# Optimization experiments

Hardware: AMD Instinct MI355X
Metric: run time of the kernel (lower is better)

Reference implementation:

```python
import jax, jax.numpy as jnp
import numpy as np

B, E, H, V, D2, T = 128, 512, 512, 32000, 1024, 17

def setup_inputs() -> dict:
    key = jax.random.key(0)
    ks = jax.random.split(key, 13)
    s = 0.02
    return {
        "features": jax.random.normal(ks[0], (B, 512), dtype=jnp.float32),
        "captions": jax.random.randint(ks[1], (B, T), 0, V, dtype=jnp.int32),
        "W_enc": jax.random.normal(ks[2], (512, E), dtype=jnp.float32) * s,
        "b_enc": jnp.zeros((E,), dtype=jnp.float32),
        "emb": jax.random.normal(ks[3], (V, E), dtype=jnp.float32) * s,
        "W_ih": jax.random.normal(ks[4], (4 * H, E), dtype=jnp.float32) * s,
        "b_ih": jnp.zeros((4 * H,), dtype=jnp.float32),
        "W_hh": jax.random.normal(ks[5], (4 * H, H), dtype=jnp.float32) * s,
        "b_hh": jnp.zeros((4 * H,), dtype=jnp.float32),
        "W_d2": jax.random.normal(ks[6], (H, D2), dtype=jnp.float32) * s,
        "b_d2": jnp.zeros((D2,), dtype=jnp.float32),
        "W_last": jax.random.normal(ks[7], (D2, V), dtype=jnp.float32) * s,
        "b_last": jnp.zeros((V,), dtype=jnp.float32),
    }


def reference(features, captions, W_enc, b_enc, emb, W_ih, b_ih, W_hh, b_hh, W_d2, b_d2, W_last, b_last):
    # encoder_last: project frozen-resnet features [B,512] -> [B,E]
    feat = features @ W_enc + b_enc
    # embed captions[:, :-1] -> [B,16,E], prepend image feature -> [B,17,E]
    e = emb[captions[:, :-1]]
    x = jnp.concatenate([feat[:, None, :], e], axis=1)  # [B,T,E]

    def step(carry, xt):
        h, c = carry
        gates = xt @ W_ih.T + b_ih + h @ W_hh.T + b_hh  # [B,4H]
        i, f, g, o = jnp.split(gates, 4, axis=-1)  # PyTorch LSTMCell gate order
        i, f, o = jax.nn.sigmoid(i), jax.nn.sigmoid(f), jax.nn.sigmoid(o)
        g = jnp.tanh(g)
        c = f * c + i * g
        h = o * jnp.tanh(c)
        return (h, c), h

    h0 = jnp.zeros((x.shape[0], H), dtype=x.dtype)
    c0 = jnp.zeros((x.shape[0], H), dtype=x.dtype)
    _, hs = jax.lax.scan(step, (h0, c0), jnp.swapaxes(x, 0, 1))  # [T,B,H]
    hs = jnp.swapaxes(hs, 0, 1)  # [B,T,H]

    out = jax.nn.relu(hs @ W_d2 + b_d2)       # [B,T,D2]
    logits = out @ W_last + b_last            # [B,T,V]
    return jax.nn.softmax(logits, axis=2)
```

## Files before the change

### kernel.cpp

```cpp
#include <hip/hip_runtime.h>
#include <hip/hip_bf16.h>

#define B_   128
#define T_   17
#define E_   512
#define H_   512
#define V_   32000
#define D2_  1024
#define MR_  (B_*T_)

typedef __attribute__((ext_vector_type(8))) short short8;
typedef __attribute__((ext_vector_type(4))) float f32x4;

__device__ __forceinline__ unsigned short f2b(float f) {
  unsigned u = __float_as_uint(f);
  u += 0x7FFFu + ((u >> 16) & 1u);
  return (unsigned short)(u >> 16);
}

__device__ __forceinline__ void async16(const void* g, void* l) {
  __builtin_amdgcn_global_load_lds((const __attribute__((address_space(1))) unsigned int*)g,
                                   (__attribute__((address_space(3))) unsigned int*)l,
                                   16, 0, 0);
}

template<int EPI>
__global__ __launch_bounds__(256, 2)
void gemm_bt(const unsigned short* __restrict__ A,
             const unsigned short* __restrict__ Bt,
             void* __restrict__ C,
             const float* __restrict__ bias0,
             const float* __restrict__ bias1,
             int N, int K)
{
  __shared__ unsigned short sA[128 * 32];
  __shared__ unsigned short sB[128 * 32];

  const int tid  = threadIdx.x;
  const int lane = tid & 63;
  const int wave = tid >> 6;
  const int wm   = wave & 1;
  const int wn   = wave >> 1;
  const size_t bm = (size_t)blockIdx.y * 128;
  const size_t bn = (size_t)blockIdx.x * 128;

  const int sRow   = wave * 32 + (lane >> 2);
  const int cpos   = lane & 3;
  const int gchunk = cpos ^ (sRow & 3);

  const unsigned short* gA  = A  + (bm + sRow)      * (size_t)K + gchunk * 8;
  const unsigned short* gA2 = A  + (bm + sRow + 16) * (size_t)K + gchunk * 8;
  const unsigned short* gB  = Bt + (bn + sRow)      * (size_t)K + gchunk * 8;
  const unsigned short* gB2 = Bt + (bn + sRow + 16) * (size_t)K + gchunk * 8;

  unsigned short* lA  = &sA[wave * 1024];
  unsigned short* lA2 = &sA[wave * 1024 + 512];
  unsigned short* lB  = &sB[wave * 1024];
  unsigned short* lB2 = &sB[wave * 1024 + 512];

  f32x4 acc[4][4] = {};

  const int fm = lane & 15;
  const int q  = lane >> 4;

  for (int kt = 0; kt < K; kt += 32) {
    async16(gA  + kt, lA);
    async16(gA2 + kt, lA2);
    async16(gB  + kt, lB);
    async16(gB2 + kt, lB2);
    __syncthreads();

    short8 af[4], bfv[4];
#pragma unroll
    for (int i = 0; i < 4; i++) {
      int ra = wm * 64 + i * 16 + fm;
      af[i]  = *(const short8*)&sA[ra * 32 + ((q ^ (ra & 3)) * 8)];
      int rb = wn * 64 + i * 16 + fm;
      bfv[i] = *(const short8*)&sB[rb * 32 + ((q ^ (rb & 3)) * 8)];
    }
#pragma unroll
    for (int i = 0; i < 4; i++)
#pragma unroll
      for (int j = 0; j < 4; j++)
        acc[i][j] = __builtin_amdgcn_mfma_f32_16x16x32_bf16(af[i], bfv[j], acc[i][j], 0, 0, 0);
    __syncthreads();
  }

#pragma unroll
  for (int i = 0; i < 4; i++) {
#pragma unroll
    for (int j = 0; j < 4; j++) {
      size_t col = bn + wn * 64 + j * 16 + fm;
      float bv = 0.f;
      if constexpr (EPI == 0) bv = bias0[col] + bias1[col];
      if constexpr (EPI == 2 || EPI == 3) bv = bias0[col];
#pragma unroll
      for (int r = 0; r < 4; r++) {
        size_t row = bm + wm * 64 + i * 16 + q * 4 + r;
        float v = acc[i][j][r] + bv;
        if constexpr (EPI == 2) {
          v = v > 0.f ? v : 0.f;
          ((unsigned short*)C)[row * N + col] = f2b(v);
        } else {
          ((float*)C)[row * N + col] = v;
        }
      }
    }
  }
}

__global__ void cvt_bf16(const float* __restrict__ src, unsigned short* __restrict__ dst, int n4) {
  int i = blockIdx.x * 256 + threadIdx.x;
  if (i >= n4) return;
  float4 v = ((const float4*)src)[i];
  ushort4 o;
  o.x = f2b(v.x); o.y = f2b(v.y); o.z = f2b(v.z); o.w = f2b(v.w);
  ((ushort4*)dst)[i] = o;
}

__global__ void transpose_cvt(const float* __restrict__ src, unsigned short* __restrict__ dst,
                              int K, int N) {
  __shared__ float tile[32][33];
  int n0 = blockIdx.x * 32, k0 = blockIdx.y * 32;
  int tcol = threadIdx.x & 31, trow = threadIdx.x >> 5;
  for (int r = trow; r < 32; r += 8)
    tile[r][tcol] = src[(size_t)(k0 + r) * N + n0 + tcol];
  __syncthreads();
  for (int r = trow; r < 32; r += 8)
    dst[(size_t)(n0 + r) * K + k0 + tcol] = f2b(tile[tcol][r]);
}

__global__ __launch_bounds__(256) void encode(const float* __restrict__ features,
                                              const float* __restrict__ W_enc,
                                              const float* __restrict__ b_enc,
                                              unsigned short* __restrict__ xb) {
  __shared__ float fs[512];
  int b = blockIdx.y, e = blockIdx.x * 256 + threadIdx.x;
  fs[threadIdx.x]       = features[b * 512 + threadIdx.x];
  fs[threadIdx.x + 256] = features[b * 512 + threadIdx.x + 256];
  __syncthreads();
  float acc = 0.f;
#pragma unroll 8
  for (int k = 0; k < 512; k++) acc += fs[k] * W_enc[(size_t)k * 512 + e];
  xb[(size_t)b * 512 + e] = f2b(acc + b_enc[e]);
}

__global__ void embed_k(const int* __restrict__ captions, const float* __restrict__ emb,
                        unsigned short* __restrict__ xb) {
  int t = blockIdx.x + 1, b = blockIdx.y;
  int tok = captions[b * T_ + (t - 1)];
  float4 v = ((const float4*)(emb + (size_t)tok * 512))[threadIdx.x];
  ushort4 o;
  o.x = f2b(v.x); o.y = f2b(v.y); o.z = f2b(v.z); o.w = f2b(v.w);
  ((ushort4*)(xb + (size_t)(t * B_ + b) * 512))[threadIdx.x] = o;
}

__global__ void lstm_point(const float* __restrict__ Gt, const float* __restrict__ lin,
                           float* __restrict__ c, unsigned short* __restrict__ hb,
                           unsigned short* __restrict__ hsb, int t, int has_lin) {
  int idx = blockIdx.x * 256 + threadIdx.x;
  int b = idx >> 9, j = idx & 511;
  const float* g = Gt + (size_t)b * 2048;
  float gi = g[j], gf = g[512 + j], gg = g[1024 + j], go = g[1536 + j];
  if (has_lin) {
    const float* l = lin + (size_t)b * 2048;
    gi += l[j]; gf += l[512 + j]; gg += l[1024 + j]; go += l[1536 + j];
  }
  float ii = 1.f / (1.f + __expf(-gi));
  float ff = 1.f / (1.f + __expf(-gf));
  float oo = 1.f / (1.f + __expf(-go));
  float gt = tanhf(gg);
  float cprev = has_lin ? c[idx] : 0.f;
  float cn = ff * cprev + ii * gt;
  float hn = oo * tanhf(cn);
  c[idx] = cn;
  unsigned short h16 = f2b(hn);
  hb[idx] = h16;
  hsb[((size_t)b * T_ + t) * 512 + j] = h16;
}

__global__ __launch_bounds__(1024) void softmax_k(float* __restrict__ out) {
  __shared__ float ps[1024];
  float* r = out + (size_t)blockIdx.x * V_;
  int tid = threadIdx.x;
  float v[32];
  float s = 0.f;
#pragma unroll
  for (int u = 0; u < 32; u++) {
    int i = u * 1024 + tid;
    if (i < V_) { float e = __expf(r[i]); v[u] = e; s += e; }
  }
  ps[tid] = s;
  __syncthreads();
  for (int o = 512; o > 0; o >>= 1) {
    if (tid < o) ps[tid] += ps[tid + o];
    __syncthreads();
  }
  float inv = 1.f / ps[0];
#pragma unroll
  for (int u = 0; u < 32; u++) {
    int i = u * 1024 + tid;
    if (i < V_) r[i] = v[u] * inv;
  }
}

extern "C" void kernel_launch(void* const* d_in, const int* in_sizes, int n_in,
                              void* d_out, int out_size, void* d_ws, size_t ws_size,
                              hipStream_t stream) {
  const float* features = (const float*)d_in[0];
  const int*   captions = (const int*)d_in[1];
  const float* W_enc  = (const float*)d_in[2];
  const float* b_enc  = (const float*)d_in[3];
  const float* emb    = (const float*)d_in[4];
  const float* W_ih   = (const float*)d_in[5];
  const float* b_ih   = (const float*)d_in[6];
  const float* W_hh   = (const float*)d_in[7];
  const float* b_hh   = (const float*)d_in[8];
  const float* W_d2   = (const float*)d_in[9];
  const float* b_d2   = (const float*)d_in[10];
  const float* W_last = (const float*)d_in[11];
  const float* b_last = (const float*)d_in[12];
  float* out = (float*)d_out;

  char* ws = (char*)d_ws;
  size_t off = 0;
  auto alloc = [&](size_t bytes) -> void* {
    void* p = ws + off;
    off += (bytes + 255) & ~(size_t)255;
    return p;
  };
  unsigned short* xb     = (unsigned short*)alloc((size_t)MR_ * E_ * 2);
  unsigned short* Wb_ih  = (unsigned short*)alloc((size_t)4 * H_ * E_ * 2);
  unsigned short* Wb_hh  = (unsigned short*)alloc((size_t)4 * H_ * H_ * 2);
  unsigned short* Wb_d2t = (unsigned short*)alloc((size_t)D2_ * H_ * 2);
  unsigned short* Wb_lt  = (unsigned short*)alloc((size_t)V_ * D2_ * 2);
  float*          G      = (float*)alloc((size_t)MR_ * 4 * H_ * 4);
  float*          lin    = (float*)alloc((size_t)B_ * 4 * H_ * 4);
  float*          cst    = (float*)alloc((size_t)B_ * H_ * 4);
  unsigned short* hb     = (unsigned short*)alloc((size_t)B_ * H_ * 2);
  unsigned short* hsb    = (unsigned short*)alloc((size_t)MR_ * H_ * 2);
  unsigned short* outb   = (unsigned short*)alloc((size_t)MR_ * D2_ * 2);
  (void)in_sizes; (void)n_in; (void)out_size; (void)ws_size;

  cvt_bf16<<<(4 * H_ * E_ / 4 + 255) / 256, 256, 0, stream>>>(W_ih, Wb_ih, 4 * H_ * E_ / 4);
  cvt_bf16<<<(4 * H_ * H_ / 4 + 255) / 256, 256, 0, stream>>>(W_hh, Wb_hh, 4 * H_ * H_ / 4);
  transpose_cvt<<<dim3(D2_ / 32, H_ / 32), 256, 0, stream>>>(W_d2, Wb_d2t, H_, D2_);
  transpose_cvt<<<dim3(V_ / 32, D2_ / 32), 256, 0, stream>>>(W_last, Wb_lt, D2_, V_);

  encode<<<dim3(2, B_), 256, 0, stream>>>(features, W_enc, b_enc, xb);
  embed_k<<<dim3(T_ - 1, B_), 128, 0, stream>>>(captions, emb, xb);

  gemm_bt<0><<<dim3(4 * H_ / 128, MR_ / 128), 256, 0, stream>>>(xb, Wb_ih, G, b_ih, b_hh, 4 * H_, E_);

  lstm_point<<<B_ * H_ / 256, 256, 0, stream>>>(G, nullptr, cst, hb, hsb, 0, 0);
  for (int t = 1; t < T_; t++) {
    gemm_bt<1><<<dim3(4 * H_ / 128, 1), 256, 0, stream>>>(hb, Wb_hh, lin, nullptr, nullptr, 4 * H_, H_);
    lstm_point<<<B_ * H_ / 256, 256, 0, stream>>>(G + (size_t)t * B_ * 4 * H_, lin, cst, hb, hsb, t, 1);
  }

  gemm_bt<2><<<dim3(D2_ / 128, MR_ / 128), 256, 0, stream>>>(hsb, Wb_d2t, outb, b_d2, nullptr, D2_, H_);

  gemm_bt<3><<<dim3(V_ / 128, MR_ / 128), 256, 0, stream>>>(outb, Wb_lt, out, b_last, nullptr, V_, D2_);

  softmax_k<<<MR_, 1024, 0, stream>>>(out);
}
```

Before: 1.022 ms.

## Fuse LSTM recurrence GEMM with cell update, interleave gates, store bf16 logits

Replaces the per-step recurrent GEMM plus pointwise kernel pair with a single fused lstm_step kernel. It uses gate-interleaved weight rows so each block computes all four gates for its hidden units, and double-buffers h. It also swaps the grid so blocks walk M fastest for weight reuse, changes the LDS swizzle, and uses a faster tanh. Logits are written as bf16 to a workspace buffer when space allows, which halves the write and read traffic of the large vocabulary output before softmax. Rounding the logits to bf16 before exp adds precision error.

```diff
diff --git a/kernel.cpp b/kernel.cpp
--- a/kernel.cpp
+++ b/kernel.cpp
@@ -16,6 +16,12 @@
   unsigned u = __float_as_uint(f);
   u += 0x7FFFu + ((u >> 16) & 1u);
   return (unsigned short)(u >> 16);
+}
+__device__ __forceinline__ float sigf(float x) { return 1.f / (1.f + __expf(-x)); }
+__device__ __forceinline__ float tanhfast(float x) {
+  x = fminf(fmaxf(x, -15.f), 15.f);
+  float e = __expf(2.f * x);
+  return (e - 1.f) / (e + 1.f);
 }
 
 __device__ __forceinline__ void async16(const void* g, void* l) {
@@ -41,12 +47,11 @@
   const int wave = tid >> 6;
   const int wm   = wave & 1;
   const int wn   = wave >> 1;
-  const size_t bm = (size_t)blockIdx.y * 128;
-  const size_t bn = (size_t)blockIdx.x * 128;
+  const size_t bm = (size_t)blockIdx.x * 128;
+  const size_t bn = (size_t)blockIdx.y * 128;
 
   const int sRow   = wave * 32 + (lane >> 2);
-  const int cpos   = lane & 3;
-  const int gchunk = cpos ^ (sRow & 3);
+  const int gchunk = (lane & 3) ^ ((sRow >> 2) & 3);
 
   const unsigned short* gA  = A  + (bm + sRow)      * (size_t)K + gchunk * 8;
   const unsigned short* gA2 = A  + (bm + sRow + 16) * (size_t)K + gchunk * 8;
@@ -59,7 +64,6 @@
   unsigned short* lB2 = &sB[wave * 1024 + 512];
 
   f32x4 acc[4][4] = {};
-
   const int fm = lane & 15;
   const int q  = lane >> 4;
 
@@ -74,9 +78,9 @@
 #pragma unroll
     for (int i = 0; i < 4; i++) {
       int ra = wm * 64 + i * 16 + fm;
-      af[i]  = *(const short8*)&sA[ra * 32 + ((q ^ (ra & 3)) * 8)];
+      af[i]  = *(const short8*)&sA[ra * 32 + ((q ^ ((ra >> 2) & 3)) * 8)];
       int rb = wn * 64 + i * 16 + fm;
-      bfv[i] = *(const short8*)&sB[rb * 32 + ((q ^ (rb & 3)) * 8)];
+      bfv[i] = *(const short8*)&sB[rb * 32 + ((q ^ ((rb >> 2) & 3)) * 8)];
     }
 #pragma unroll
     for (int i = 0; i < 4; i++)
@@ -92,8 +96,11 @@
     for (int j = 0; j < 4; j++) {
       size_t col = bn + wn * 64 + j * 16 + fm;
       float bv = 0.f;
-      if constexpr (EPI == 0) bv = bias0[col] + bias1[col];
-      if constexpr (EPI == 2 || EPI == 3) bv = bias0[col];
+      if constexpr (EPI == 0) {
+        size_t oc = ((col & 3) << 9) + (col >> 2);
+        bv = bias0[oc] + bias1[oc];
+      }
+      if constexpr (EPI == 2 || EPI == 3 || EPI == 4) bv = bias0[col];
 #pragma unroll
       for (int r = 0; r < 4; r++) {
         size_t row = bm + wm * 64 + i * 16 + q * 4 + r;
@@ -101,6 +108,8 @@
         if constexpr (EPI == 2) {
           v = v > 0.f ? v : 0.f;
           ((unsigned short*)C)[row * N + col] = f2b(v);
+        } else if constexpr (EPI == 3) {
+          ((unsigned short*)C)[row * N + col] = f2b(v);
         } else {
           ((float*)C)[row * N + col] = v;
         }
@@ -109,13 +118,113 @@
   }
 }
 
-__global__ void cvt_bf16(const float* __restrict__ src, unsigned short* __restrict__ dst, int n4) {
-  int i = blockIdx.x * 256 + threadIdx.x;
-  if (i >= n4) return;
-  float4 v = ((const float4*)src)[i];
+__global__ __launch_bounds__(256)
+void lstm_step(const unsigned short* __restrict__ hprev,
+               const unsigned short* __restrict__ Whh,
+               const float* __restrict__ Gt,
+               float* __restrict__ c,
+               unsigned short* __restrict__ hout,
+               unsigned short* __restrict__ hsb,
+               int t)
+{
+  __shared__ float gl[128 * 132];
+  unsigned short* sA = (unsigned short*)gl;
+  unsigned short* sB = (unsigned short*)(gl + 4096);
+
+  const int tid  = threadIdx.x;
+  const int lane = tid & 63;
+  const int wave = tid >> 6;
+  const int wm   = wave & 1;
+  const int wn   = wave >> 1;
+  const int n0   = blockIdx.x * 128;
+
+  const int sR  = lane >> 3;
+  const int gch = (lane & 7) ^ sR;
+  const size_t aoff = (size_t)(wave * 32 + sR) * 512 + gch * 8;
+  const size_t boff = (size_t)(n0 + wave * 32 + sR) * 512 + gch * 8;
+
+  f32x4 acc[4][4] = {};
+  const int fm = lane & 15;
+  const int q  = lane >> 4;
+
+  for (int kt = 0; kt < 512; kt += 64) {
+#pragma unroll
+    for (int s = 0; s < 4; s++) {
+      async16(hprev + aoff + s * 4096 + kt, sA + wave * 2048 + s * 512);
+      async16(Whh   + boff + s * 4096 + kt, sB + wave * 2048 + s * 512);
+    }
+    __syncthreads();
+
+    short8 af[2][4], bfv[2][4];
+#pragma unroll
+    for (int kk = 0; kk < 2; kk++) {
+      int cch = kk * 4 + q;
+#pragma unroll
+      for (int i = 0; i < 4; i++) {
+        int ra = wm * 64 + i * 16 + fm;
+        af[kk][i]  = *(const short8*)&sA[ra * 64 + ((cch ^ (ra & 7)) * 8)];
+        int rb = wn * 64 + i * 16 + fm;
+        bfv[kk][i] = *(const short8*)&sB[rb * 64 + ((cch ^ (rb & 7)) * 8)];
+      }
+    }
+#pragma unroll
+    for (int kk = 0; kk < 2; kk++)
+#pragma unroll
+      for (int i = 0; i < 4; i++)
+#pragma unroll
+        for (int j = 0; j < 4; j++)
+          acc[i][j] = __builtin_amdgcn_mfma_f32_16x16x32_bf16(af[kk][i], bfv[kk][j], acc[i][j], 0, 0, 0);
+    __syncthreads();
+  }
+
+#pragma unroll
+  for (int i = 0; i < 4; i++)
+#pragma unroll
+    for (int j = 0; j < 4; j++)
+#pragma unroll
+      for (int r = 0; r < 4; r++)
+        gl[(wm * 64 + i * 16 + q * 4 + r) * 132 + wn * 64 + j * 16 + fm] = acc[i][j][r];
+  __syncthreads();
+
+#pragma unroll
+  for (int it = 0; it < 16; it++) {
+    int p   = it * 256 + tid;
+    int row = p >> 5;
+    int ul  = p & 31;
+    float4 a4 = *(float4*)&gl[row * 132 + ul * 4];
+    float4 G4 = *(const float4*)&Gt[row * 2048 + n0 + ul * 4];
+    float gi = a4.x + G4.x, gf = a4.y + G4.y, gg = a4.z + G4.z, go = a4.w + G4.w;
+    int gu  = (n0 >> 2) + ul;
+    int idx = row * 512 + gu;
+    float cn = sigf(gf) * c[idx] + sigf(gi) * tanhfast(gg);
+    c[idx] = cn;
+    float hn = sigf(go) * tanhfast(cn);
+    unsigned short h16 = f2b(hn);
+    hout[idx] = h16;
+    hsb[((size_t)row * T_ + t) * 512 + gu] = h16;
+  }
+}
+
+__global__ void lstm_point0(const float* __restrict__ G0, float* __restrict__ c,
+                            unsigned short* __restrict__ hb, unsigned short* __restrict__ hsb) {
+  int idx = blockIdx.x * 256 + threadIdx.x;
+  int b = idx >> 9, u = idx & 511;
+  float4 g4 = ((const float4*)(G0 + (size_t)b * 2048))[u];
+  float cn = sigf(g4.x) * tanhfast(g4.z);
+  c[idx] = cn;
+  float hn = sigf(g4.w) * tanhfast(cn);
+  unsigned short h16 = f2b(hn);
+  hb[idx] = h16;
+  hsb[((size_t)b * T_ + 0) * 512 + u] = h16;
+}
+
+__global__ void permute_cvt(const float* __restrict__ src, unsigned short* __restrict__ dst) {
+  int p  = blockIdx.x;
+  int ir = ((p & 3) << 9) + (p >> 2);
+  float4 v = ((const float4*)(src + (size_t)ir * 512))[threadIdx.x];
   ushort4 o;
   o.x = f2b(v.x); o.y = f2b(v.y); o.z = f2b(v.z); o.w = f2b(v.w);
-  ((ushort4*)dst)[i] = o;
+  ((ushort4*)(dst + (size_t)p * 512))[threadIdx.x] = o;
 }
 
 __global__ void transpose_cvt(const float* __restrict__ src, unsigned short* __restrict__ dst,
@@ -155,31 +264,50 @@
   ((ushort4*)(xb + (size_t)(t * B_ + b) * 512))[threadIdx.x] = o;
 }
 
-__global__ void lstm_point(const float* __restrict__ Gt, const float* __restrict__ lin,
-                           float* __restrict__ c, unsigned short* __restrict__ hb,
-                           unsigned short* __restrict__ hsb, int t, int has_lin) {
-  int idx = blockIdx.x * 256 + threadIdx.x;
-  int b = idx >> 9, j = idx & 511;
-  const float* g = Gt + (size_t)b * 2048;
-  float gi = g[j], gf = g[512 + j], gg = g[1024 + j], go = g[1536 + j];
-  if (has_lin) {
-    const float* l = lin + (size_t)b * 2048;
-    gi += l[j]; gf += l[512 + j]; gg += l[1024 + j]; go += l[1536 + j];
-  }
-  float ii = 1.f / (1.f + __expf(-gi));
-  float ff = 1.f / (1.f + __expf(-gf));
-  float oo = 1.f / (1.f + __expf(-go));
-  float gt = tanhf(gg);
-  float cprev = has_lin ? c[idx] : 0.f;
-  float cn = ff * cprev + ii * gt;
-  float hn = oo * tanhf(cn);
-  c[idx] = cn;
-  unsigned short h16 = f2b(hn);
-  hb[idx] = h16;
-  hsb[((size_t)b * T_ + t) * 512 + j] = h16;
-}
-
-__global__ __launch_bounds__(1024) void softmax_k(float* __restrict__ out) {
+__global__ __launch_bounds__(1024) void softmax_b(const unsigned short* __restrict__ lg,
+                                                  float* __restrict__ out) {
+  __shared__ float ps[1024];
+  const uint4* r4 = (const uint4*)(lg + (size_t)blockIdx.x * V_);
+  float* orow = out + (size_t)blockIdx.x * V_;
+  int tid = threadIdx.x;
+  float v[4][8];
+  float s = 0.f;
+#pragma unroll
+  for (int u = 0; u < 4; u++) {
+    int i = u * 1024 + tid;
+    if (i < 4000) {
+      uint4 w = r4[i];
+      unsigned a[4] = {w.x, w.y, w.z, w.w};
+#pragma unroll
+      for (int k = 0; k < 4; k++) {
+        float lo = __uint_as_float(a[k] << 16);
+        float hi = __uint_as_float(a[k] & 0xffff0000u);
+        float e0 = __expf(lo), e1 = __expf(hi);
+        v[u][2 * k] = e0; v[u][2 * k + 1] = e1;
+        s += e0 + e1;
+      }
+    }
+  }
+  ps[tid] = s;
+  __syncthreads();
+  for (int o = 512; o > 0; o >>= 1) {
+    if (tid < o) ps[tid] += ps[tid + o];
+    __syncthreads();
+  }
+  float inv = 1.f / ps[0];
+#pragma unroll
+  for (int u = 0; u < 4; u++) {
+    int i = u * 1024 + tid;
+    if (i < 4000) {
+      float4 o1 = {v[u][0] * inv, v[u][1] * inv, v[u][2] * inv, v[u][3] * inv};
+      float4 o2 = {v[u][4] * inv, v[u][5] * inv, v[u][6] * inv, v[u][7] * inv};
+      ((float4*)(orow + (size_t)i * 8))[0] = o1;
+      ((float4*)(orow + (size_t)i * 8))[1] = o2;
+    }
+  }
+}
+
+__global__ __launch_bounds__(1024) void softmax_f(float* __restrict__ out) {
   __shared__ float ps[1024];
   float* r = out + (size_t)blockIdx.x * V_;
   int tid = threadIdx.x;
@@ -235,32 +363,41 @@
   unsigned short* Wb_d2t = (unsigned short*)alloc((size_t)D2_ * H_ * 2);
   unsigned short* Wb_lt  = (unsigned short*)alloc((size_t)V_ * D2_ * 2);
   float*          G      = (float*)alloc((size_t)MR_ * 4 * H_ * 4);
-  float*          lin    = (float*)alloc((size_t)B_ * 4 * H_ * 4);
   float*          cst    = (float*)alloc((size_t)B_ * H_ * 4);
-  unsigned short* hb     = (unsigned short*)alloc((size_t)B_ * H_ * 2);
+  unsigned short* hb0    = (unsigned short*)alloc((size_t)B_ * H_ * 2);
+  unsigned short* hb1    = (unsigned short*)alloc((size_t)B_ * H_ * 2);
   unsigned short* hsb    = (unsigned short*)alloc((size_t)MR_ * H_ * 2);
   unsigned short* outb   = (unsigned short*)alloc((size_t)MR_ * D2_ * 2);
-  (void)in_sizes; (void)n_in; (void)out_size; (void)ws_size;
-
-  cvt_bf16<<<(4 * H_ * E_ / 4 + 255) / 256, 256, 0, stream>>>(W_ih, Wb_ih, 4 * H_ * E_ / 4);
-  cvt_bf16<<<(4 * H_ * H_ / 4 + 255) / 256, 256, 0, stream>>>(W_hh, Wb_hh, 4 * H_ * H_ / 4);
+  size_t off_base = off;
+  unsigned short* lgb    = (unsigned short*)alloc((size_t)MR_ * V_ * 2);
+  const bool bf16_logits = (off <= ws_size);
+  (void)in_sizes; (void)n_in; (void)out_size; (void)off_base;
+
+  permute_cvt<<<2048, 128, 0, stream>>>(W_ih, Wb_ih);
+  permute_cvt<<<2048, 128, 0, stream>>>(W_hh, Wb_hh);
   transpose_cvt<<<dim3(D2_ / 32, H_ / 32), 256, 0, stream>>>(W_d2, Wb_d2t, H_, D2_);
-  transpose_cvt<<<dim3(V_ / 32, D2_ / 32), 256, 0, stream>>>(W_last, Wb_lt, D2_, V_);
 
   encode<<<dim3(2, B_), 256, 0, stream>>>(features, W_enc, b_enc, xb);
   embed_k<<<dim3(T_ - 1, B_), 128, 0, stream>>>(captions, emb, xb);
 
-  gemm_bt<0><<<dim3(4 * H_ / 128, MR_ / 128), 256, 0, stream>>>(xb, Wb_ih, G, b_ih, b_hh, 4 * H_, E_);
-
-  lstm_point<<<B_ * H_ / 256, 256, 0, stream>>>(G, nullptr, cst, hb, hsb, 0, 0);
+  gemm_bt<0><<<dim3(MR_ / 128, 4 * H_ / 128), 256, 0, stream>>>(xb, Wb_ih, G, b_ih, b_hh, 4 * H_, E_);
+
+  lstm_point0<<<B_ * H_ / 256, 256, 0, stream>>>(G, cst, hb0, hsb);
   for (int t = 1; t < T_; t++) {
-    gemm_bt<1><<<dim3(4 * H_ / 128, 1), 256, 0, stream>>>(hb, Wb_hh, lin, nullptr, nullptr, 4 * H_, H_);
-    lstm_point<<<B_ * H_ / 256, 256, 0, stream>>>(G + (size_t)t * B_ * 4 * H_, lin, cst, hb, hsb, t, 1);
-  }
-
-  gemm_bt<2><<<dim3(D2_ / 128, MR_ / 128), 256, 0, stream>>>(hsb, Wb_d2t, outb, b_d2, nullptr, D2_, H_);
-
-  gemm_bt<3><<<dim3(V_ / 128, MR_ / 128), 256, 0, stream>>>(outb, Wb_lt, out, b_last, nullptr, V_, D2_);
-
-  softmax_k<<<MR_, 1024, 0, stream>>>(out);
-}
+    unsigned short* hp = (t & 1) ? hb0 : hb1;
+    unsigned short* hc = (t & 1) ? hb1 : hb0;
+    lstm_step<<<16, 256, 0, stream>>>(hp, Wb_hh, G + (size_t)t * B_ * 4 * H_, cst, hc, hsb, t);
+  }
+
+  transpose_cvt<<<dim3(V_ / 32, D2_ / 32), 256, 0, stream>>>(W_last, Wb_lt, D2_, V_);
+
+  gemm_bt<2><<<dim3(MR_ / 128, D2_ / 128), 256, 0, stream>>>(hsb, Wb_d2t, outb, b_d2, nullptr, D2_, H_);
+
+  if (bf16_logits) {
+    gemm_bt<3><<<dim3(MR_ / 128, V_ / 128), 256, 0, stream>>>(outb, Wb_lt, lgb, b_last, nullptr, V_, D2_);
+    softmax_b<<<MR_, 1024, 0, stream>>>(lgb, out);
+  } else {
+    gemm_bt<4><<<dim3(MR_ / 128, V_ / 128), 256, 0, stream>>>(outb, Wb_lt, out, b_last, nullptr, V_, D2_);
+    softmax_f<<<MR_, 1024, 0, stream>>>(out);
+  }
+}
```

Result: faster. 973.2 us (-4.8%).
